# Optimization experiments

Hardware: AMD Instinct MI355X
Metric: run time of the kernel (lower is better)

The kernel has to match this reference:

```python
import jax, jax.numpy as jnp
import numpy as np

B, V, T, D, H = 8, 64, 256, 256, 8
DH = D // H
LN_EPS = 1e-5


def setup_inputs() -> dict:
    key = jax.random.key(0)
    k0, k1, k2, k3 = jax.random.split(key, 4)
    x = jax.random.normal(k0, (B, V, T + 1, D), dtype=jnp.float32)
    obs_mask = jax.random.randint(k1, (B, V, T), 0, 2).astype(bool)
    ln_w = jnp.ones((D,), jnp.float32)
    ln_b = jnp.zeros((D,), jnp.float32)
    w_qkv = jax.random.normal(k2, (3 * D, D), dtype=jnp.float32) * 0.02   # torch Linear weight (out,in), no bias
    w_proj = jax.random.normal(k3, (D, D), dtype=jnp.float32) * 0.02
    b_proj = jnp.zeros((D,), jnp.float32)
    return dict(x=x, obs_mask=obs_mask, ln_w=ln_w, ln_b=ln_b,
                w_qkv=w_qkv, w_proj=w_proj, b_proj=b_proj)


def reference(x, obs_mask, ln_w, ln_b, w_qkv, w_proj, b_proj):
    b, v, t1, d = x.shape
    h, dh = H, D // H

    # LayerNorm over last dim
    mu = jnp.mean(x, axis=-1, keepdims=True)
    var = jnp.mean(jnp.square(x - mu), axis=-1, keepdims=True)
    xn = (x - mu) * jax.lax.rsqrt(var + LN_EPS) * ln_w + ln_b

    # QKV projection: (B,V,T1,3D) -> (B,V,T1,3,H,dh)
    qkv = jnp.einsum('bvtd,ed->bvte', xn, w_qkv).reshape(b, v, t1, 3, h, dh)
    qf = qkv[:, :, :, 0]  # (B,V,T1,H,dh)
    kf = qkv[:, :, :, 1]
    vf = qkv[:, :, :, 2]

    # Queries from position 0 only: (B,H,V,dh)
    q = jnp.transpose(qf[:, :, 0], (0, 2, 1, 3))

    # Keys: masked mean over time (query token at pos 0 always observed)
    mask = jnp.concatenate([jnp.ones((b, v, 1), bool), obs_mask], axis=2)  # (B,V,T1)
    mf = mask[..., None, None].astype(kf.dtype)                            # (B,V,T1,1,1)
    cnt = jnp.clip(mask.sum(axis=2).astype(kf.dtype), 1.0)[:, :, None, None]
    k = (kf * mf).sum(axis=2) / cnt                                        # (B,V,H,dh)
    k = jnp.transpose(k, (0, 2, 1, 3))                                     # (B,H,V,dh)

    # Small cross-variable attention matrix (B,H,V,V)
    scale = dh ** -0.5
    attn = jax.nn.softmax(jnp.einsum('bhqd,bhkd->bhqk', q, k) * scale, axis=-1)

    # Values packed with temporal structure: (B,H,V,dh,T1)
    vp = jnp.transpose(vf, (0, 3, 1, 4, 2))
    out = jnp.einsum('bhqk,bhkdt->bhqdt', attn, vp)                        # (B,H,V,dh,T1)

    # Unpack back to (B,V,T1,D)
    out = jnp.transpose(out, (0, 2, 4, 1, 3)).reshape(b, v, t1, d)
    out = out @ w_proj.T + b_proj
    return x + out
```

## Files before the change

kernel.cpp:

```cpp
#include <hip/hip_runtime.h>
#include <hip/hip_bf16.h>

typedef unsigned short u16;
typedef __attribute__((ext_vector_type(8))) short short8;
typedef __attribute__((ext_vector_type(4))) float f32x4;

#define B_ 8
#define V_ 64
#define T_ 256
#define T1_ 257
#define D_ 256
#define H_ 8
#define DH_ 32

__device__ __forceinline__ u16 f2bf(float f){
  union { float f; unsigned int u; } v; v.f = f;
  unsigned int u = v.u;
  return (u16)((u + 0x7fffu + ((u >> 16) & 1u)) >> 16);
}

__global__ void k0_conv(const float* __restrict__ wqkv, const float* __restrict__ wproj,
                        u16* __restrict__ wv, u16* __restrict__ wp){
  int i = blockIdx.x * 256 + threadIdx.x;
  if (i < 65536) wv[i] = f2bf(wqkv[131072 + i]);
  else           wp[i - 65536] = f2bf(wproj[i - 65536]);
}

__global__ void k_zero(float* __restrict__ p, int n){
  int i = blockIdx.x * blockDim.x + threadIdx.x;
  if (i < n) p[i] = 0.f;
}

__global__ void k1_ln(const float* __restrict__ x, const int* __restrict__ mask,
                      const float* __restrict__ lnw, const float* __restrict__ lnb,
                      float* __restrict__ musig, float* __restrict__ xsum){
  int bv = blockIdx.x;
  int tid = threadIdx.x;
  int lane = tid & 63, wid = tid >> 6;
  int t0 = blockIdx.y * 65;
  int tend = t0 + 65; if (tend > T1_) tend = T1_;
  __shared__ float xsred[4][D_];
  float4 w4 = *(const float4*)&lnw[lane * 4];
  float4 b4 = *(const float4*)&lnb[lane * 4];
  float xs0 = 0.f, xs1 = 0.f, xs2 = 0.f, xs3 = 0.f;
  for (int t = t0 + wid; t < tend; t += 4){
    float4 v = *(const float4*)&x[((long)bv * T1_ + t) * D_ + lane * 4];
    float s  = v.x + v.y + v.z + v.w;
    float s2 = v.x*v.x + v.y*v.y + v.z*v.z + v.w*v.w;
    #pragma unroll
    for (int off = 1; off < 64; off <<= 1){
      s  += __shfl_xor(s,  off, 64);
      s2 += __shfl_xor(s2, off, 64);
    }
    float mu   = s * (1.f / 256.f);
    float var  = s2 * (1.f / 256.f) - mu * mu;
    float rstd = rsqrtf(var + 1e-5f);
    if (lane == 0){
      musig[((long)bv * T1_ + t) * 2]     = mu;
      musig[((long)bv * T1_ + t) * 2 + 1] = rstd;
    }
    int m = (t == 0) ? 1 : mask[bv * T_ + (t - 1)];
    if (m){
      xs0 += (v.x - mu) * rstd * w4.x + b4.x;
      xs1 += (v.y - mu) * rstd * w4.y + b4.y;
      xs2 += (v.z - mu) * rstd * w4.z + b4.z;
      xs3 += (v.w - mu) * rstd * w4.w + b4.w;
    }
  }
  xsred[wid][lane * 4]     = xs0;
  xsred[wid][lane * 4 + 1] = xs1;
  xsred[wid][lane * 4 + 2] = xs2;
  xsred[wid][lane * 4 + 3] = xs3;
  __syncthreads();
  float r = xsred[0][tid] + xsred[1][tid] + xsred[2][tid] + xsred[3][tid];
  atomicAdd(&xsum[bv * D_ + tid], r);
}

__global__ void k2a_qk(const float* __restrict__ x, const int* __restrict__ mask,
                       const float* __restrict__ lnw, const float* __restrict__ lnb,
                       const float* __restrict__ wqkv,
                       const float* __restrict__ musig, const float* __restrict__ xsum,
                       float* __restrict__ qout, float* __restrict__ kout){
  int bv = blockIdx.x, tid = threadIdx.x;
  int lane = tid & 63, wid = tid >> 6;
  __shared__ __align__(16) float xn0[D_];
  __shared__ __align__(16) float xs[D_];
  __shared__ float redc[4];
  int s = mask[bv * T_ + tid];
  #pragma unroll
  for (int off = 32; off >= 1; off >>= 1) s += __shfl_down(s, off, 64);
  if (lane == 0) redc[wid] = (float)s;
  __syncthreads();
  float cnt = 1.f + redc[0] + redc[1] + redc[2] + redc[3];
  float mu = musig[((long)bv * T1_) * 2], rstd = musig[((long)bv * T1_) * 2 + 1];
  xn0[tid] = (x[((long)bv * T1_) * D_ + tid] - mu) * rstd * lnw[tid] + lnb[tid];
  xs[tid]  = xsum[bv * D_ + tid] * (1.f / cnt);
  __syncthreads();
  float4 xq = *(const float4*)&xn0[lane * 4];
  float4 xk = *(const float4*)&xs[lane * 4];
  int e0 = (blockIdx.y * 4 + wid) * 16;
  for (int i = 0; i < 16; ++i){
    int e = e0 + i;
    float4 wq4 = *(const float4*)&wqkv[(long)e * D_ + lane * 4];
    float4 wk4 = *(const float4*)&wqkv[(long)(256 + e) * D_ + lane * 4];
    float sq = xq.x*wq4.x + xq.y*wq4.y + xq.z*wq4.z + xq.w*wq4.w;
    float sk = xk.x*wk4.x + xk.y*wk4.y + xk.z*wk4.z + xk.w*wk4.w;
    #pragma unroll
    for (int off = 32; off >= 1; off >>= 1){
      sq += __shfl_down(sq, off, 64);
      sk += __shfl_down(sk, off, 64);
    }
    if (lane == 0){ qout[bv * D_ + e] = sq; kout[bv * D_ + e] = sk; }
  }
}

__global__ void k2b_attn(const float* __restrict__ q, const float* __restrict__ k,
                         u16* __restrict__ attn){
  int bh = blockIdx.x; int b = bh >> 3, h = bh & 7;
  int tid = threadIdx.x;
  __shared__ float qs[64][DH_], ks[64][DH_];
  for (int d = 0; d < DH_; ++d){
    qs[tid][d] = q[((long)(b * V_ + tid)) * D_ + h * DH_ + d];
    ks[tid][d] = k[((long)(b * V_ + tid)) * D_ + h * DH_ + d];
  }
  __syncthreads();
  const float scale = 0.17677669529663687f;
  float sc[64];
  float mx = -1e30f;
  #pragma unroll
  for (int j = 0; j < 64; ++j){
    float a = 0.f;
    #pragma unroll
    for (int d = 0; d < DH_; ++d) a += qs[tid][d] * ks[j][d];
    a *= scale; sc[j] = a; mx = fmaxf(mx, a);
  }
  float sum = 0.f;
  #pragma unroll
  for (int j = 0; j < 64; ++j){ float e = __expf(sc[j] - mx); sc[j] = e; sum += e; }
  float inv = 1.f / sum;
  #pragma unroll
  for (int j = 0; j < 64; ++j) attn[((long)bh * 64 + tid) * 64 + j] = f2bf(sc[j] * inv);
}

__global__ __launch_bounds__(512, 4) void k3_main(
    const float* __restrict__ x, const float* __restrict__ lnw, const float* __restrict__ lnb,
    const float* __restrict__ bproj, const float* __restrict__ musig,
    const u16* __restrict__ wv, const u16* __restrict__ wp,
    const u16* __restrict__ attn, float* __restrict__ out){
  constexpr int XS = 264;
  constexpr int VS = 72;
  __shared__ __align__(16) u16 Xs[64 * XS];
  __shared__ __align__(16) u16 VT[D_ * VS];
  __shared__ float lnw_s[D_], lnb_s[D_], bp_s[D_];
  __shared__ float ms_s[V_ * 2];

  int bt = blockIdx.x; int b = bt / T1_, t = bt % T1_;
  int tid = threadIdx.x;
  int w = tid >> 6, lane = tid & 63, lm = lane & 15, lq = lane >> 4;
  int cw = w * 32;

  if (tid < 256){ lnw_s[tid] = lnw[tid]; lnb_s[tid] = lnb[tid]; bp_s[tid] = bproj[tid]; }
  else if (tid < 384){
    int i = tid - 256;
    ms_s[i] = musig[(((long)b * V_ + (i >> 1)) * T1_ + t) * 2 + (i & 1)];
  }
  __syncthreads();

  #pragma unroll
  for (int i = 0; i < 4; ++i){
    int seg = i * 512 + tid;
    int vr = seg >> 5;
    int c8 = (seg & 31) * 8;
    const float* gp = x + (((long)b * V_ + vr) * T1_ + t) * D_ + c8;
    float4 a0 = *(const float4*)gp;
    float4 a1 = *(const float4*)(gp + 4);
    float mu = ms_s[vr * 2], rs = ms_s[vr * 2 + 1];
    float av[8] = {a0.x, a0.y, a0.z, a0.w, a1.x, a1.y, a1.z, a1.w};
    union { u16 us[8]; uint4 q; } pk;
    #pragma unroll
    for (int j = 0; j < 8; ++j)
      pk.us[j] = f2bf((av[j] - mu) * rs * lnw_s[c8 + j] + lnb_s[c8 + j]);
    *(uint4*)&Xs[vr * XS + c8] = pk.q;
  }
  __syncthreads();

  f32x4 acc1[4][2];
  #pragma unroll
  for (int mt = 0; mt < 4; ++mt)
    #pragma unroll
    for (int nt = 0; nt < 2; ++nt) acc1[mt][nt] = (f32x4){0.f, 0.f, 0.f, 0.f};
  for (int kk = 0; kk < 8; ++kk){
    short8 af[4], bfr[2];
    #pragma unroll
    for (int mt = 0; mt < 4; ++mt)
      af[mt] = *(const short8*)&Xs[(mt * 16 + lm) * XS + kk * 32 + lq * 8];
    #pragma unroll
    for (int nt = 0; nt < 2; ++nt)
      bfr[nt] = *(const short8*)&wv[(long)(cw + nt * 16 + lm) * D_ + kk * 32 + lq * 8];
    #pragma unroll
    for (int mt = 0; mt < 4; ++mt)
      #pragma unroll
      for (int nt = 0; nt < 2; ++nt)
        acc1[mt][nt] = __builtin_amdgcn_mfma_f32_16x16x32_bf16(af[mt], bfr[nt], acc1[mt][nt], 0, 0, 0);
  }
  #pragma unroll
  for (int mt = 0; mt < 4; ++mt)
    #pragma unroll
    for (int nt = 0; nt < 2; ++nt){
      int col = cw + nt * 16 + lm;
      int row = mt * 16 + lq * 4;
      union { u16 us[4]; uint2 q; } pv;
      #pragma unroll
      for (int r = 0; r < 4; ++r) pv.us[r] = f2bf(acc1[mt][nt][r]);
      *(uint2*)&VT[col * VS + row] = pv.q;
    }
  __syncthreads();

  int h = w;
  f32x4 acc2[4][2];
  #pragma unroll
  for (int mt = 0; mt < 4; ++mt)
    #pragma unroll
    for (int nt = 0; nt < 2; ++nt) acc2[mt][nt] = (f32x4){0.f, 0.f, 0.f, 0.f};
  #pragma unroll
  for (int kk = 0; kk < 2; ++kk){
    short8 af[4], bfr[2];
    #pragma unroll
    for (int mt = 0; mt < 4; ++mt)
      af[mt] = *(const short8*)&attn[((long)(b * H_ + h) * 64 + mt * 16 + lm) * 64 + kk * 32 + lq * 8];
    #pragma unroll
    for (int nt = 0; nt < 2; ++nt)
      bfr[nt] = *(const short8*)&VT[(h * 32 + nt * 16 + lm) * VS + kk * 32 + lq * 8];
    #pragma unroll
    for (int mt = 0; mt < 4; ++mt)
      #pragma unroll
      for (int nt = 0; nt < 2; ++nt)
        acc2[mt][nt] = __builtin_amdgcn_mfma_f32_16x16x32_bf16(af[mt], bfr[nt], acc2[mt][nt], 0, 0, 0);
  }
  #pragma unroll
  for (int mt = 0; mt < 4; ++mt)
    #pragma unroll
    for (int nt = 0; nt < 2; ++nt){
      int col = h * 32 + nt * 16 + lm;
      #pragma unroll
      for (int r = 0; r < 4; ++r){
        int row = mt * 16 + lq * 4 + r;
        Xs[row * XS + col] = f2bf(acc2[mt][nt][r]);
      }
    }
  __syncthreads();

  f32x4 acc3[4][2];
  #pragma unroll
  for (int mt = 0; mt < 4; ++mt)
    #pragma unroll
    for (int nt = 0; nt < 2; ++nt) acc3[mt][nt] = (f32x4){0.f, 0.f, 0.f, 0.f};
  for (int kk = 0; kk < 8; ++kk){
    short8 af[4], bfr[2];
    #pragma unroll
    for (int mt = 0; mt < 4; ++mt)
      af[mt] = *(const short8*)&Xs[(mt * 16 + lm) * XS + kk * 32 + lq * 8];
    #pragma unroll
    for (int nt = 0; nt < 2; ++nt)
      bfr[nt] = *(const short8*)&wp[(long)(cw + nt * 16 + lm) * D_ + kk * 32 + lq * 8];
    #pragma unroll
    for (int mt = 0; mt < 4; ++mt)
      #pragma unroll
      for (int nt = 0; nt < 2; ++nt)
        acc3[mt][nt] = __builtin_amdgcn_mfma_f32_16x16x32_bf16(af[mt], bfr[nt], acc3[mt][nt], 0, 0, 0);
  }
  #pragma unroll
  for (int mt = 0; mt < 4; ++mt)
    #pragma unroll
    for (int nt = 0; nt < 2; ++nt){
      int e = cw + nt * 16 + lm;
      #pragma unroll
      for (int r = 0; r < 4; ++r){
        int vr = mt * 16 + lq * 4 + r;
        long g = (((long)b * V_ + vr) * T1_ + t) * D_ + e;
        out[g] = acc3[mt][nt][r] + bp_s[e] + x[g];
      }
    }
}

extern "C" void kernel_launch(void* const* d_in, const int* in_sizes, int n_in,
                              void* d_out, int out_size, void* d_ws, size_t ws_size,
                              hipStream_t stream){
  const float* x     = (const float*)d_in[0];
  const int*   mask  = (const int*)d_in[1];
  const float* lnw   = (const float*)d_in[2];
  const float* lnb   = (const float*)d_in[3];
  const float* wqkv  = (const float*)d_in[4];
  const float* wproj = (const float*)d_in[5];
  const float* bproj = (const float*)d_in[6];
  float* out = (float*)d_out;
  char* ws = (char*)d_ws;
  float* musig = (float*)(ws);
  float* xsum  = (float*)(ws + 1052672);
  float* qbuf  = (float*)(ws + 1576960);
  float* kbuf  = (float*)(ws + 2101248);
  u16*   attn  = (u16*)  (ws + 2625536);
  u16*   wv    = (u16*)  (ws + 3149824);
  u16*   wp    = (u16*)  (ws + 3280896);

  k0_conv<<<512, 256, 0, stream>>>(wqkv, wproj, wv, wp);
  k_zero<<<512, 256, 0, stream>>>(xsum, 131072);
  k1_ln<<<dim3(512, 4), 256, 0, stream>>>(x, mask, lnw, lnb, musig, xsum);
  k2a_qk<<<dim3(512, 4), 256, 0, stream>>>(x, mask, lnw, lnb, wqkv, musig, xsum, qbuf, kbuf);
  k2b_attn<<<64, 64, 0, stream>>>(qbuf, kbuf, attn);
  k3_main<<<B_ * T1_, 512, 0, stream>>>(x, lnw, lnb, bproj, musig, wv, wp, attn, out);
}
```

Measured before the change: 405.9 us.

## Fold weight conversion into LN kernel, drop atomics, alias LDS buffers in main kernel

```diff
diff --git a/kernel.cpp b/kernel.cpp
--- a/kernel.cpp
+++ b/kernel.cpp
@@ -19,25 +19,21 @@
   return (u16)((u + 0x7fffu + ((u >> 16) & 1u)) >> 16);
 }
 
-__global__ void k0_conv(const float* __restrict__ wqkv, const float* __restrict__ wproj,
-                        u16* __restrict__ wv, u16* __restrict__ wp){
-  int i = blockIdx.x * 256 + threadIdx.x;
-  if (i < 65536) wv[i] = f2bf(wqkv[131072 + i]);
-  else           wp[i - 65536] = f2bf(wproj[i - 65536]);
-}
-
-__global__ void k_zero(float* __restrict__ p, int n){
-  int i = blockIdx.x * blockDim.x + threadIdx.x;
-  if (i < n) p[i] = 0.f;
-}
-
 __global__ void k1_ln(const float* __restrict__ x, const int* __restrict__ mask,
                       const float* __restrict__ lnw, const float* __restrict__ lnb,
-                      float* __restrict__ musig, float* __restrict__ xsum){
+                      const float* __restrict__ wqkv, const float* __restrict__ wproj,
+                      float* __restrict__ musig, float* __restrict__ xsump,
+                      u16* __restrict__ wv, u16* __restrict__ wp){
   int bv = blockIdx.x;
+  int y = blockIdx.y;
   int tid = threadIdx.x;
   int lane = tid & 63, wid = tid >> 6;
-  int t0 = blockIdx.y * 65;
+  if (tid < 64){
+    int i = (y * 512 + bv) * 64 + tid;
+    if (i < 65536) wv[i] = f2bf(wqkv[131072 + i]);
+    else           wp[i - 65536] = f2bf(wproj[i - 65536]);
+  }
+  int t0 = y * 65;
   int tend = t0 + 65; if (tend > T1_) tend = T1_;
   __shared__ float xsred[4][D_];
   float4 w4 = *(const float4*)&lnw[lane * 4];
@@ -73,13 +69,13 @@
   xsred[wid][lane * 4 + 3] = xs3;
   __syncthreads();
   float r = xsred[0][tid] + xsred[1][tid] + xsred[2][tid] + xsred[3][tid];
-  atomicAdd(&xsum[bv * D_ + tid], r);
+  xsump[((long)bv * 4 + y) * D_ + tid] = r;
 }
 
 __global__ void k2a_qk(const float* __restrict__ x, const int* __restrict__ mask,
                        const float* __restrict__ lnw, const float* __restrict__ lnb,
                        const float* __restrict__ wqkv,
-                       const float* __restrict__ musig, const float* __restrict__ xsum,
+                       const float* __restrict__ musig, const float* __restrict__ xsump,
                        float* __restrict__ qout, float* __restrict__ kout){
   int bv = blockIdx.x, tid = threadIdx.x;
   int lane = tid & 63, wid = tid >> 6;
@@ -94,7 +90,9 @@
   float cnt = 1.f + redc[0] + redc[1] + redc[2] + redc[3];
   float mu = musig[((long)bv * T1_) * 2], rstd = musig[((long)bv * T1_) * 2 + 1];
   xn0[tid] = (x[((long)bv * T1_) * D_ + tid] - mu) * rstd * lnw[tid] + lnb[tid];
-  xs[tid]  = xsum[bv * D_ + tid] * (1.f / cnt);
+  float ps = xsump[((long)bv * 4) * D_ + tid] + xsump[((long)bv * 4 + 1) * D_ + tid]
+           + xsump[((long)bv * 4 + 2) * D_ + tid] + xsump[((long)bv * 4 + 3) * D_ + tid];
+  xs[tid] = ps * (1.f / cnt);
   __syncthreads();
   float4 xq = *(const float4*)&xn0[lane * 4];
   float4 xk = *(const float4*)&xs[lane * 4];
@@ -142,16 +140,14 @@
   for (int j = 0; j < 64; ++j) attn[((long)bh * 64 + tid) * 64 + j] = f2bf(sc[j] * inv);
 }
 
-__global__ __launch_bounds__(512, 4) void k3_main(
+__global__ __launch_bounds__(512, 8) void k3_main(
     const float* __restrict__ x, const float* __restrict__ lnw, const float* __restrict__ lnb,
     const float* __restrict__ bproj, const float* __restrict__ musig,
     const u16* __restrict__ wv, const u16* __restrict__ wp,
     const u16* __restrict__ attn, float* __restrict__ out){
   constexpr int XS = 264;
   constexpr int VS = 72;
-  __shared__ __align__(16) u16 Xs[64 * XS];
-  __shared__ __align__(16) u16 VT[D_ * VS];
-  __shared__ float lnw_s[D_], lnb_s[D_], bp_s[D_];
+  __shared__ __align__(16) u16 buf[256 * VS];
   __shared__ float ms_s[V_ * 2];
 
   int bt = blockIdx.x; int b = bt / T1_, t = bt % T1_;
@@ -159,28 +155,32 @@
   int w = tid >> 6, lane = tid & 63, lm = lane & 15, lq = lane >> 4;
   int cw = w * 32;
 
-  if (tid < 256){ lnw_s[tid] = lnw[tid]; lnb_s[tid] = lnb[tid]; bp_s[tid] = bproj[tid]; }
-  else if (tid < 384){
-    int i = tid - 256;
-    ms_s[i] = musig[(((long)b * V_ + (i >> 1)) * T1_ + t) * 2 + (i & 1)];
-  }
+  if (tid < 128)
+    ms_s[tid] = musig[(((long)b * V_ + (tid >> 1)) * T1_ + t) * 2 + (tid & 1)];
+  int c8 = (tid & 31) * 8;
+  float4 lw0 = *(const float4*)&lnw[c8];
+  float4 lw1 = *(const float4*)&lnw[c8 + 4];
+  float4 lb0 = *(const float4*)&lnb[c8];
+  float4 lb1 = *(const float4*)&lnb[c8 + 4];
   __syncthreads();
 
   #pragma unroll
   for (int i = 0; i < 4; ++i){
-    int seg = i * 512 + tid;
-    int vr = seg >> 5;
-    int c8 = (seg & 31) * 8;
+    int vr = (i * 512 + tid) >> 5;
     const float* gp = x + (((long)b * V_ + vr) * T1_ + t) * D_ + c8;
     float4 a0 = *(const float4*)gp;
     float4 a1 = *(const float4*)(gp + 4);
     float mu = ms_s[vr * 2], rs = ms_s[vr * 2 + 1];
-    float av[8] = {a0.x, a0.y, a0.z, a0.w, a1.x, a1.y, a1.z, a1.w};
     union { u16 us[8]; uint4 q; } pk;
-    #pragma unroll
-    for (int j = 0; j < 8; ++j)
-      pk.us[j] = f2bf((av[j] - mu) * rs * lnw_s[c8 + j] + lnb_s[c8 + j]);
-    *(uint4*)&Xs[vr * XS + c8] = pk.q;
+    pk.us[0] = f2bf((a0.x - mu) * rs * lw0.x + lb0.x);
+    pk.us[1] = f2bf((a0.y - mu) * rs * lw0.y + lb0.y);
+    pk.us[2] = f2bf((a0.z - mu) * rs * lw0.z + lb0.z);
+    pk.us[3] = f2bf((a0.w - mu) * rs * lw0.w + lb0.w);
+    pk.us[4] = f2bf((a1.x - mu) * rs * lw1.x + lb1.x);
+    pk.us[5] = f2bf((a1.y - mu) * rs * lw1.y + lb1.y);
+    pk.us[6] = f2bf((a1.z - mu) * rs * lw1.z + lb1.z);
+    pk.us[7] = f2bf((a1.w - mu) * rs * lw1.w + lb1.w);
+    *(uint4*)&buf[vr * XS + c8] = pk.q;
   }
   __syncthreads();
 
@@ -193,7 +193,7 @@
     short8 af[4], bfr[2];
     #pragma unroll
     for (int mt = 0; mt < 4; ++mt)
-      af[mt] = *(const short8*)&Xs[(mt * 16 + lm) * XS + kk * 32 + lq * 8];
+      af[mt] = *(const short8*)&buf[(mt * 16 + lm) * XS + kk * 32 + lq * 8];
     #pragma unroll
     for (int nt = 0; nt < 2; ++nt)
       bfr[nt] = *(const short8*)&wv[(long)(cw + nt * 16 + lm) * D_ + kk * 32 + lq * 8];
@@ -203,6 +203,8 @@
       for (int nt = 0; nt < 2; ++nt)
         acc1[mt][nt] = __builtin_amdgcn_mfma_f32_16x16x32_bf16(af[mt], bfr[nt], acc1[mt][nt], 0, 0, 0);
   }
+  __syncthreads();
+
   #pragma unroll
   for (int mt = 0; mt < 4; ++mt)
     #pragma unroll
@@ -212,9 +214,8 @@
       union { u16 us[4]; uint2 q; } pv;
       #pragma unroll
       for (int r = 0; r < 4; ++r) pv.us[r] = f2bf(acc1[mt][nt][r]);
-      *(uint2*)&VT[col * VS + row] = pv.q;
-    }
-  __syncthreads();
+      *(uint2*)&buf[col * VS + row] = pv.q;
+    }
 
   int h = w;
   f32x4 acc2[4][2];
@@ -230,22 +231,24 @@
       af[mt] = *(const short8*)&attn[((long)(b * H_ + h) * 64 + mt * 16 + lm) * 64 + kk * 32 + lq * 8];
     #pragma unroll
     for (int nt = 0; nt < 2; ++nt)
-      bfr[nt] = *(const short8*)&VT[(h * 32 + nt * 16 + lm) * VS + kk * 32 + lq * 8];
+      bfr[nt] = *(const short8*)&buf[(cw + nt * 16 + lm) * VS + kk * 32 + lq * 8];
     #pragma unroll
     for (int mt = 0; mt < 4; ++mt)
       #pragma unroll
       for (int nt = 0; nt < 2; ++nt)
         acc2[mt][nt] = __builtin_amdgcn_mfma_f32_16x16x32_bf16(af[mt], bfr[nt], acc2[mt][nt], 0, 0, 0);
   }
+  __syncthreads();
+
   #pragma unroll
   for (int mt = 0; mt < 4; ++mt)
     #pragma unroll
     for (int nt = 0; nt < 2; ++nt){
-      int col = h * 32 + nt * 16 + lm;
+      int col = cw + nt * 16 + lm;
       #pragma unroll
       for (int r = 0; r < 4; ++r){
         int row = mt * 16 + lq * 4 + r;
-        Xs[row * XS + col] = f2bf(acc2[mt][nt][r]);
+        buf[row * XS + col] = f2bf(acc2[mt][nt][r]);
       }
     }
   __syncthreads();
@@ -259,7 +262,7 @@
     short8 af[4], bfr[2];
     #pragma unroll
     for (int mt = 0; mt < 4; ++mt)
-      af[mt] = *(const short8*)&Xs[(mt * 16 + lm) * XS + kk * 32 + lq * 8];
+      af[mt] = *(const short8*)&buf[(mt * 16 + lm) * XS + kk * 32 + lq * 8];
     #pragma unroll
     for (int nt = 0; nt < 2; ++nt)
       bfr[nt] = *(const short8*)&wp[(long)(cw + nt * 16 + lm) * D_ + kk * 32 + lq * 8];
@@ -269,16 +272,19 @@
       for (int nt = 0; nt < 2; ++nt)
         acc3[mt][nt] = __builtin_amdgcn_mfma_f32_16x16x32_bf16(af[mt], bfr[nt], acc3[mt][nt], 0, 0, 0);
   }
+  float bpa = bproj[cw + lm];
+  float bpb = bproj[cw + 16 + lm];
   #pragma unroll
   for (int mt = 0; mt < 4; ++mt)
     #pragma unroll
     for (int nt = 0; nt < 2; ++nt){
       int e = cw + nt * 16 + lm;
+      float bp = nt ? bpb : bpa;
       #pragma unroll
       for (int r = 0; r < 4; ++r){
         int vr = mt * 16 + lq * 4 + r;
         long g = (((long)b * V_ + vr) * T1_ + t) * D_ + e;
-        out[g] = acc3[mt][nt][r] + bp_s[e] + x[g];
+        out[g] = acc3[mt][nt][r] + bp + x[g];
       }
     }
 }
@@ -296,17 +302,15 @@
   float* out = (float*)d_out;
   char* ws = (char*)d_ws;
   float* musig = (float*)(ws);
-  float* xsum  = (float*)(ws + 1052672);
-  float* qbuf  = (float*)(ws + 1576960);
-  float* kbuf  = (float*)(ws + 2101248);
-  u16*   attn  = (u16*)  (ws + 2625536);
-  u16*   wv    = (u16*)  (ws + 3149824);
-  u16*   wp    = (u16*)  (ws + 3280896);
-
-  k0_conv<<<512, 256, 0, stream>>>(wqkv, wproj, wv, wp);
-  k_zero<<<512, 256, 0, stream>>>(xsum, 131072);
-  k1_ln<<<dim3(512, 4), 256, 0, stream>>>(x, mask, lnw, lnb, musig, xsum);
-  k2a_qk<<<dim3(512, 4), 256, 0, stream>>>(x, mask, lnw, lnb, wqkv, musig, xsum, qbuf, kbuf);
+  float* xsump = (float*)(ws + 1052672);
+  float* qbuf  = (float*)(ws + 3149824);
+  float* kbuf  = (float*)(ws + 3674112);
+  u16*   attn  = (u16*)  (ws + 4198400);
+  u16*   wv    = (u16*)  (ws + 4722688);
+  u16*   wp    = (u16*)  (ws + 4853760);
+
+  k1_ln<<<dim3(512, 4), 256, 0, stream>>>(x, mask, lnw, lnb, wqkv, wproj, musig, xsump, wv, wp);
+  k2a_qk<<<dim3(512, 4), 256, 0, stream>>>(x, mask, lnw, lnb, wqkv, musig, xsump, qbuf, kbuf);
   k2b_attn<<<64, 64, 0, stream>>>(qbuf, kbuf, attn);
   k3_main<<<B_ * T1_, 512, 0, stream>>>(x, lnw, lnb, bproj, musig, wv, wp, attn, out);
 }
```

After: 426.0 us. 4.9% more time.
